# Optimization experiments

Measured on AMD Instinct MI355X. Metric: run time of the kernel, lower is better.

Reference implementation:

```python
import jax, jax.numpy as jnp
import numpy as np

D_MODEL = 1024
NUM_HEADS = 16
D_LATENT = 256
HEAD_DIM = D_MODEL // NUM_HEADS
B, S = 4, 2048


def setup_inputs() -> dict:
    key = jax.random.key(0)
    ks = jax.random.split(key, 11)
    sc_m = 1.0 / np.sqrt(D_MODEL)
    sc_l = 1.0 / np.sqrt(D_LATENT)
    return {
        "x": jax.random.normal(ks[0], (B, S, D_MODEL), dtype=jnp.float32),
        # weights stored as (in, out); equivalent to torch Linear with W^T
        "Wc": jax.random.normal(ks[1], (D_MODEL, D_LATENT), dtype=jnp.float32) * sc_m,
        "bc": jax.random.normal(ks[2], (D_LATENT,), dtype=jnp.float32) * sc_m,
        "Wk": jax.random.normal(ks[3], (D_LATENT, D_MODEL), dtype=jnp.float32) * sc_l,
        "bk": jax.random.normal(ks[4], (D_MODEL,), dtype=jnp.float32) * sc_l,
        "Wv": jax.random.normal(ks[5], (D_LATENT, D_MODEL), dtype=jnp.float32) * sc_l,
        "bv": jax.random.normal(ks[6], (D_MODEL,), dtype=jnp.float32) * sc_l,
        "Wq": jax.random.normal(ks[7], (D_MODEL, D_MODEL), dtype=jnp.float32) * sc_m,
        "bq": jax.random.normal(ks[8], (D_MODEL,), dtype=jnp.float32) * sc_m,
        "Wo": jax.random.normal(ks[9], (D_MODEL, D_MODEL), dtype=jnp.float32) * sc_m,
        "bo": jax.random.normal(ks[10], (D_MODEL,), dtype=jnp.float32) * sc_m,
    }


def reference(x, Wc, bc, Wk, bk, Wv, bv, Wq, bq, Wo, bo):
    b, s, _ = x.shape
    Q = x @ Wq + bq                       # [b,s,d_model]
    kv_latent = x @ Wc + bc               # [b,s,d_latent]
    K = kv_latent @ Wk + bk               # [b,s,d_model]
    V = kv_latent @ Wv + bv               # [b,s,d_model]
    # split heads -> [b,h,s,hd]
    Q = Q.reshape(b, s, NUM_HEADS, HEAD_DIM).transpose(0, 2, 1, 3)
    K = K.reshape(b, s, NUM_HEADS, HEAD_DIM).transpose(0, 2, 1, 3)
    V = V.reshape(b, s, NUM_HEADS, HEAD_DIM).transpose(0, 2, 1, 3)
    scores = jnp.einsum("bhqd,bhkd->bhqk", Q, K) / np.sqrt(HEAD_DIM)
    attn = jax.nn.softmax(scores, axis=-1)  # dropout p=0.0 (eval) -> identity
    out = jnp.einsum("bhqk,bhkd->bhqd", attn, V)
    out = out.transpose(0, 2, 1, 3).reshape(b, s, D_MODEL)
    return out @ Wo + bo
```

## Files before the change

kernel.cpp:

```cpp
#include <hip/hip_runtime.h>

typedef __bf16 bf16;
typedef __bf16 bf16x4 __attribute__((ext_vector_type(4)));
typedef __bf16 bf16x8 __attribute__((ext_vector_type(8)));
typedef float f32x4 __attribute__((ext_vector_type(4)));

#define NHEADS 16
#define HDIM 64
#define SEQ 2048
#define BATCH 4
#define DMODEL 1024
#define NTOK (BATCH * SEQ)
#define KVBLK 64
#define QSCALE 0.18033688f
#define C0EXP  -28.853901f

typedef void gvoid __attribute__((address_space(1)));
typedef void lvoid __attribute__((address_space(3)));

__device__ __forceinline__ f32x4 mfma16(bf16x8 a, bf16x8 b, f32x4 c) {
  return __builtin_amdgcn_mfma_f32_16x16x32_bf16(a, b, c, 0, 0, 0);
}

__device__ __forceinline__ void gload16(const bf16* g, bf16* l) {
  __builtin_amdgcn_global_load_lds((gvoid*)g, (lvoid*)l, 16, 0, 0);
}

__global__ __launch_bounds__(256) void cvt_f32_bf16(
    const float* __restrict__ in, bf16* __restrict__ out, long n) {
  const long i = ((long)blockIdx.x * 256 + threadIdx.x) * 8;
  if (i >= n) return;
  const float4 a = *(const float4*)(in + i);
  const float4 b = *(const float4*)(in + i + 4);
  bf16x8 o;
  o[0] = (bf16)a.x; o[1] = (bf16)a.y; o[2] = (bf16)a.z; o[3] = (bf16)a.w;
  o[4] = (bf16)b.x; o[5] = (bf16)b.y; o[6] = (bf16)b.z; o[7] = (bf16)b.w;
  *(bf16x8*)(out + i) = o;
}

__global__ __launch_bounds__(256) void transpose_cvt(
    const float* __restrict__ in, bf16* __restrict__ out, int K, int N) {
  __shared__ float t[32][33];
  const int n0 = blockIdx.x * 32, k0 = blockIdx.y * 32;
  for (int i = threadIdx.y; i < 32; i += 8)
    t[i][threadIdx.x] = in[(long)(k0 + i) * N + n0 + threadIdx.x];
  __syncthreads();
  for (int i = threadIdx.y; i < 32; i += 8)
    out[(long)(n0 + i) * K + k0 + threadIdx.x] = (bf16)t[threadIdx.x][i];
}

template <int MODE, typename OutT>
__global__ __launch_bounds__(256) void gemm_bt(
    const bf16* __restrict__ A, const bf16* __restrict__ Bt,
    const float* __restrict__ bias, const float* __restrict__ bias2,
    OutT* __restrict__ D, bf16* __restrict__ D2, int N, int K) {
  __shared__ bf16 As[3][128 * 32];
  __shared__ bf16 Bs[3][128 * 32];
  const int tid = threadIdx.x;
  const int lane = tid & 63;
  const int wave = tid >> 6;
  const int wr = (wave >> 1) * 64;
  const int wc = (wave & 1) * 64;
  const int r16 = lane & 15;
  const int kg = lane >> 4;
  const long rowBase = (long)blockIdx.x * 128;
  const long colBase = (long)blockIdx.y * 128;

  const int o0 = tid * 16;
  const int o1 = o0 + 4096;
  const int ra0 = o0 >> 6, ra1 = o1 >> 6;
  const int ca0 = ((o0 & 63) ^ (((ra0 >> 1) & 3) << 4)) >> 1;
  const int ca1 = ((o1 & 63) ^ (((ra1 >> 1) & 3) << 4)) >> 1;
  const bf16* pA0 = A + (rowBase + ra0) * K + ca0;
  const bf16* pA1 = A + (rowBase + ra1) * K + ca1;
  const bf16* pB0 = Bt + (colBase + ra0) * K + ca0;
  const bf16* pB1 = Bt + (colBase + ra1) * K + ca1;
  const int e0 = o0 >> 1, e1 = o1 >> 1;

  auto gaddr = [](const bf16* base, int row, int bytecol) -> const bf16* {
    return base + row * 32 + ((bytecol ^ (((row >> 1) & 3) << 4)) >> 1);
  };

  f32x4 acc[4][4] = {};
  const int nk = K >> 5;

#define GSTAGE(kt_)                                        \
  {                                                        \
    const int b_ = (kt_) % 3;                              \
    const int o_ = (kt_) * 32;                             \
    gload16(pA0 + o_, &As[b_][e0]);                        \
    gload16(pA1 + o_, &As[b_][e1]);                        \
    gload16(pB0 + o_, &Bs[b_][e0]);                        \
    gload16(pB1 + o_, &Bs[b_][e1]);                        \
  }

  GSTAGE(0);
  GSTAGE(1);
  asm volatile("s_waitcnt vmcnt(4)" ::: "memory");
  asm volatile("s_barrier" ::: "memory");

  for (int kt = 0; kt < nk; ++kt) {
    if (kt + 2 < nk) {
      GSTAGE(kt + 2);
      asm volatile("s_waitcnt vmcnt(4)" ::: "memory");
    } else {
      asm volatile("s_waitcnt vmcnt(0)" ::: "memory");
    }
    const bf16* as = As[kt % 3];
    const bf16* bs = Bs[kt % 3];
    bf16x8 af[4], bfr[4];
#pragma unroll
    for (int m = 0; m < 4; ++m)
      af[m] = *(const bf16x8*)gaddr(as, wr + m * 16 + r16, kg * 16);
#pragma unroll
    for (int n = 0; n < 4; ++n)
      bfr[n] = *(const bf16x8*)gaddr(bs, wc + n * 16 + r16, kg * 16);
    __builtin_amdgcn_s_setprio(1);
#pragma unroll
    for (int m = 0; m < 4; ++m)
#pragma unroll
      for (int n = 0; n < 4; ++n)
        acc[m][n] = mfma16(af[m], bfr[n], acc[m][n]);
    __builtin_amdgcn_s_setprio(0);
    asm volatile("s_barrier" ::: "memory");
  }
#undef GSTAGE

#pragma unroll
  for (int n = 0; n < 4; ++n) {
    const long col = colBase + wc + n * 16 + r16;
    const bool primary = (MODE == 0) || (col < 1024);
    const float bvv = primary ? bias[col] : bias2[col - 1024];
#pragma unroll
    for (int m = 0; m < 4; ++m) {
      const long row0 = rowBase + wr + m * 16 + kg * 4;
#pragma unroll
      for (int r = 0; r < 4; ++r) {
        const long row = row0 + r;
        float v = acc[m][n][r] + bvv;
        if (MODE == 0) {
          D[row * N + col] = (OutT)v;
        } else {
          const long b = row >> 11, s = row & (SEQ - 1);
          if (MODE == 3) {
            if (primary) {
              const long h = col >> 6, d = col & 63;
              D[((b * NHEADS + h) * SEQ + s) * HDIM + d] = (OutT)(v * QSCALE);
            } else {
              D2[row * 256 + (col - 1024)] = (bf16)v;
            }
          } else {
            if (primary) {
              const long h = col >> 6, d = col & 63;
              D[((b * NHEADS + h) * SEQ + s) * HDIM + d] = (OutT)v;
            } else {
              const long c2 = col - 1024;
              const long h = c2 >> 6, d = c2 & 63;
              D2[((b * NHEADS + h) * HDIM + d) * SEQ + s] = (bf16)v;
            }
          }
        }
      }
    }
  }
}

__global__ __launch_bounds__(512, 4) void mla_attn(
    const bf16* __restrict__ Q, const bf16* __restrict__ Kg,
    const bf16* __restrict__ Vt, bf16* __restrict__ Out) {
  __shared__ bf16 Kl[3][KVBLK * HDIM];
  __shared__ bf16 Vl[3][HDIM * KVBLK];
  __shared__ bf16 Pl[8][32][64];
  const int tid = threadIdx.x;
  const int lane = tid & 63;
  const int w = tid >> 6;
  const int r16 = lane & 15;
  const int kg = lane >> 4;
  const int bid = (int)blockIdx.x;
  const int lb = (bid & 7) * 64 + (bid >> 3);
  const int qb = lb & 7;
  const int bh = lb >> 3;
  const bf16* Qp = Q + (long)bh * SEQ * HDIM;
  const bf16* Kp = Kg + (long)bh * SEQ * HDIM;
  const bf16* Vp = Vt + (long)bh * HDIM * SEQ;
  const int q0 = qb * 256 + w * 32;

  const int so = tid * 16;
  const int srow = so >> 7;
  const int scol = ((so & 127) ^ ((srow & 7) << 4)) >> 1;
  const bf16* KgS = Kp + (long)srow * HDIM + scol;
  const bf16* VgS = Vp + (long)srow * SEQ + scol;
  const int se = so >> 1;

  bf16x8 aq[2][2];
#pragma unroll
  for (int qm = 0; qm < 2; ++qm) {
    const bf16* qp = Qp + (long)(q0 + qm * 16 + r16) * HDIM + kg * 8;
    aq[qm][0] = *(const bf16x8*)qp;
    aq[qm][1] = *(const bf16x8*)(qp + 32);
  }

  bf16x8 kones;
#pragma unroll
  for (int j = 0; j < 8; ++j) kones[j] = (bf16)1.0f;

  f32x4 accO[2][4];
  f32x4 lsumv[2] = {{0.f, 0.f, 0.f, 0.f}, {0.f, 0.f, 0.f, 0.f}};
#pragma unroll
  for (int qm = 0; qm < 2; ++qm)
#pragma unroll
    for (int dt = 0; dt < 4; ++dt) accO[qm][dt] = (f32x4){0.f, 0.f, 0.f, 0.f};
  const f32x4 c0v = {C0EXP, C0EXP, C0EXP, C0EXP};

  auto kaddr = [](const bf16* base, int row, int bytecol) -> const bf16* {
    return base + row * 64 + ((bytecol ^ ((row & 7) << 4)) >> 1);
  };

#define ASTAGE(t_)                                                   \
  {                                                                  \
    const int b_ = (t_) % 3;                                         \
    const long off_ = (long)(t_) * KVBLK;                            \
    gload16(KgS + off_ * HDIM, (bf16*)Kl[b_] + se);                  \
    gload16(VgS + off_, (bf16*)Vl[b_] + se);                         \
  }

  ASTAGE(0);
  ASTAGE(1);
  asm volatile("s_waitcnt vmcnt(2)" ::: "memory");
  asm volatile("s_barrier" ::: "memory");

  const int NT = SEQ / KVBLK;
  for (int t = 0; t < NT; ++t) {
    if (t + 2 < NT) {
      ASTAGE(t + 2);
      asm volatile("s_waitcnt vmcnt(2)" ::: "memory");
    } else {
      asm volatile("s_waitcnt vmcnt(0)" ::: "memory");
    }
    const bf16* kl = Kl[t % 3];
    const bf16* vl = Vl[t % 3];
    f32x4 sc[2][4];
    __builtin_amdgcn_s_setprio(1);
#pragma unroll
    for (int kt = 0; kt < 4; ++kt) {
      const int row = kt * 16 + r16;
      const bf16x8 kf0 = *(const bf16x8*)kaddr(kl, row, kg * 16);
      const bf16x8 kf1 = *(const bf16x8*)kaddr(kl, row, 64 + kg * 16);
#pragma unroll
      for (int qm = 0; qm < 2; ++qm) {
        f32x4 tv = mfma16(kf0, aq[qm][0], c0v);
        tv = mfma16(kf1, aq[qm][1], tv);
        sc[qm][kt] = tv;
      }
    }
    __builtin_amdgcn_s_setprio(0);
#pragma unroll
    for (int qm = 0; qm < 2; ++qm) {
      bf16* prow = &Pl[w][qm * 16 + r16][0];
      const int sw = (r16 & 7) << 4;
#pragma unroll
      for (int kt = 0; kt < 4; ++kt) {
        bf16x4 pk;
#pragma unroll
        for (int r = 0; r < 4; ++r)
          pk[r] = (bf16)__builtin_amdgcn_exp2f(sc[qm][kt][r]);
        *(bf16x4*)((char*)prow + ((kt * 32 + kg * 8) ^ sw)) = pk;
      }
    }
    __builtin_amdgcn_s_setprio(1);
#pragma unroll
    for (int kc = 0; kc < 2; ++kc) {
      bf16x8 ap[2];
#pragma unroll
      for (int qm = 0; qm < 2; ++qm) {
        const bf16* prow = &Pl[w][qm * 16 + r16][0];
        const int sw = (r16 & 7) << 4;
        ap[qm] = *(const bf16x8*)((const char*)prow + ((kc * 64 + kg * 16) ^ sw));
      }
      lsumv[0] = mfma16(ap[0], kones, lsumv[0]);
      lsumv[1] = mfma16(ap[1], kones, lsumv[1]);
#pragma unroll
      for (int dt = 0; dt < 4; ++dt) {
        const int vrow = dt * 16 + r16;
        const bf16x8 vf = *(const bf16x8*)kaddr(vl, vrow, kc * 64 + kg * 16);
        accO[0][dt] = mfma16(ap[0], vf, accO[0][dt]);
        accO[1][dt] = mfma16(ap[1], vf, accO[1][dt]);
      }
    }
    __builtin_amdgcn_s_setprio(0);
    asm volatile("s_barrier" ::: "memory");
  }
#undef ASTAGE

  const int b = bh >> 4, h = bh & 15;
#pragma unroll
  for (int qm = 0; qm < 2; ++qm)
#pragma unroll
    for (int r = 0; r < 4; ++r) {
      const float inv = 1.f / lsumv[qm][r];
      const long qrow = q0 + qm * 16 + kg * 4 + r;
      bf16* op = Out + ((long)b * SEQ + qrow) * DMODEL + h * HDIM;
#pragma unroll
      for (int dt = 0; dt < 4; ++dt)
        op[dt * 16 + r16] = (bf16)(accO[qm][dt][r] * inv);
    }
}

extern "C" void kernel_launch(void* const* d_in, const int* in_sizes, int n_in,
                              void* d_out, int out_size, void* d_ws, size_t ws_size,
                              hipStream_t stream) {
  const float* x  = (const float*)d_in[0];
  const float* Wc = (const float*)d_in[1];
  const float* bc = (const float*)d_in[2];
  const float* Wk = (const float*)d_in[3];
  const float* bk = (const float*)d_in[4];
  const float* Wv = (const float*)d_in[5];
  const float* bv = (const float*)d_in[6];
  const float* Wq = (const float*)d_in[7];
  const float* bq = (const float*)d_in[8];
  const float* Wo = (const float*)d_in[9];
  const float* bo = (const float*)d_in[10];
  float* out = (float*)d_out;

  bf16* p = (bf16*)d_ws;
  bf16* xb   = p; p += (long)NTOK * 1024;
  bf16* WqcT = p; p += 1280 * 1024;
  bf16* WkvT = p; p += 2048 * 256;
  bf16* WoT  = p; p += 1024 * 1024;
  bf16* Qb   = p; p += (long)NTOK * 1024;
  bf16* Kb   = p; p += (long)NTOK * 1024;
  bf16* Vtb  = p; p += (long)NTOK * 1024;
  bf16* Cb   = p; p += (long)NTOK * 256;
  bf16* AO   = xb;

  cvt_f32_bf16<<<(long)NTOK * 1024 / (256 * 8), 256, 0, stream>>>(x, xb, (long)NTOK * 1024);

  dim3 tt(32, 8);
  transpose_cvt<<<dim3(32, 32), tt, 0, stream>>>(Wq, WqcT, 1024, 1024);
  transpose_cvt<<<dim3(8, 32),  tt, 0, stream>>>(Wc, WqcT + 1024 * 1024, 1024, 256);
  transpose_cvt<<<dim3(32, 8),  tt, 0, stream>>>(Wk, WkvT, 256, 1024);
  transpose_cvt<<<dim3(32, 8),  tt, 0, stream>>>(Wv, WkvT + 1024 * 256, 256, 1024);
  transpose_cvt<<<dim3(32, 32), tt, 0, stream>>>(Wo, WoT, 1024, 1024);

  gemm_bt<3, bf16><<<dim3(64, 10), 256, 0, stream>>>(xb, WqcT, bq, bc, Qb, Cb, 1280, 1024);
  gemm_bt<4, bf16><<<dim3(64, 16), 256, 0, stream>>>(Cb, WkvT, bk, bv, Kb, Vtb, 2048, 256);

  mla_attn<<<(SEQ / 256) * BATCH * NHEADS, 512, 0, stream>>>(Qb, Kb, Vtb, AO);

  gemm_bt<0, float><<<dim3(64, 8), 256, 0, stream>>>(AO, WoT, bo, bo, out, (bf16*)nullptr, 1024, 1024);
}
```

Before: 186.2 us.

## Stage GEMM epilogue through LDS for coalesced stores; sum softmax in registers

The GEMM epilogue for the head-split modes now writes the bias-added tile into shared memory (transposed for the V-transpose output) and then issues coalesced 16-byte row stores, replacing scattered 2-byte global writes. The attention kernel drops the MFMA-with-ones row-sum and instead accumulates fp32 exp values per lane, reducing across lanes with shuffles at the end. This cuts uncoalesced write traffic and MFMA work, at the cost of an extra barrier and LDS pass in the epilogue. The row sum now uses unrounded fp32 values rather than bf16-rounded ones, so the normalization differs slightly.

```diff
diff --git a/kernel.cpp b/kernel.cpp
--- a/kernel.cpp
+++ b/kernel.cpp
@@ -54,8 +54,9 @@
     const bf16* __restrict__ A, const bf16* __restrict__ Bt,
     const float* __restrict__ bias, const float* __restrict__ bias2,
     OutT* __restrict__ D, bf16* __restrict__ D2, int N, int K) {
-  __shared__ bf16 As[3][128 * 32];
-  __shared__ bf16 Bs[3][128 * 32];
+  __shared__ bf16 smem[3 * 4096 * 2];
+  bf16* const AsB = smem;
+  bf16* const BsB = smem + 3 * 4096;
   const int tid = threadIdx.x;
   const int lane = tid & 63;
   const int wave = tid >> 6;
@@ -88,10 +89,10 @@
   {                                                        \
     const int b_ = (kt_) % 3;                              \
     const int o_ = (kt_) * 32;                             \
-    gload16(pA0 + o_, &As[b_][e0]);                        \
-    gload16(pA1 + o_, &As[b_][e1]);                        \
-    gload16(pB0 + o_, &Bs[b_][e0]);                        \
-    gload16(pB1 + o_, &Bs[b_][e1]);                        \
+    gload16(pA0 + o_, AsB + b_ * 4096 + e0);               \
+    gload16(pA1 + o_, AsB + b_ * 4096 + e1);               \
+    gload16(pB0 + o_, BsB + b_ * 4096 + e0);               \
+    gload16(pB1 + o_, BsB + b_ * 4096 + e1);               \
   }
 
   GSTAGE(0);
@@ -106,8 +107,8 @@
     } else {
       asm volatile("s_waitcnt vmcnt(0)" ::: "memory");
     }
-    const bf16* as = As[kt % 3];
-    const bf16* bs = Bs[kt % 3];
+    const bf16* as = AsB + (kt % 3) * 4096;
+    const bf16* bs = BsB + (kt % 3) * 4096;
     bf16x8 af[4], bfr[4];
 #pragma unroll
     for (int m = 0; m < 4; ++m)
@@ -126,42 +127,64 @@
   }
 #undef GSTAGE
 
-#pragma unroll
-  for (int n = 0; n < 4; ++n) {
-    const long col = colBase + wc + n * 16 + r16;
-    const bool primary = (MODE == 0) || (col < 1024);
-    const float bvv = primary ? bias[col] : bias2[col - 1024];
-#pragma unroll
-    for (int m = 0; m < 4; ++m) {
-      const long row0 = rowBase + wr + m * 16 + kg * 4;
-#pragma unroll
-      for (int r = 0; r < 4; ++r) {
-        const long row = row0 + r;
-        float v = acc[m][n][r] + bvv;
-        if (MODE == 0) {
-          D[row * N + col] = (OutT)v;
-        } else {
-          const long b = row >> 11, s = row & (SEQ - 1);
-          if (MODE == 3) {
-            if (primary) {
-              const long h = col >> 6, d = col & 63;
-              D[((b * NHEADS + h) * SEQ + s) * HDIM + d] = (OutT)(v * QSCALE);
-            } else {
-              D2[row * 256 + (col - 1024)] = (bf16)v;
-            }
-          } else {
-            if (primary) {
-              const long h = col >> 6, d = col & 63;
-              D[((b * NHEADS + h) * SEQ + s) * HDIM + d] = (OutT)v;
-            } else {
-              const long c2 = col - 1024;
-              const long h = c2 >> 6, d = c2 & 63;
-              D2[((b * NHEADS + h) * HDIM + d) * SEQ + s] = (bf16)v;
-            }
-          }
+  if (MODE == 0) {
+#pragma unroll
+    for (int n = 0; n < 4; ++n) {
+      const long col = colBase + wc + n * 16 + r16;
+      const float bvv = bias[col];
+#pragma unroll
+      for (int m = 0; m < 4; ++m) {
+        const long row0 = rowBase + wr + m * 16 + kg * 4;
+#pragma unroll
+        for (int r = 0; r < 4; ++r)
+          D[(row0 + r) * N + col] = (OutT)(acc[m][n][r] + bvv);
+      }
+    }
+  } else {
+    const bool tr = (MODE == 4) && (colBase >= 1024);
+    bf16* E = smem;
+#pragma unroll
+    for (int n = 0; n < 4; ++n) {
+      const int cl = wc + n * 16 + r16;
+      const long col = colBase + cl;
+      const bool primary = col < 1024;
+      const float bvv = primary ? bias[col] : bias2[col - 1024];
+#pragma unroll
+      for (int m = 0; m < 4; ++m) {
+#pragma unroll
+        for (int r = 0; r < 4; ++r) {
+          const int rl = wr + m * 16 + kg * 4 + r;
+          float v = acc[m][n][r] + bvv;
+          if (MODE == 3 && primary) v *= QSCALE;
+          if (tr) E[cl * 136 + rl] = (bf16)v;
+          else    E[rl * 136 + cl] = (bf16)v;
         }
       }
     }
+    __syncthreads();
+    const int er = tid >> 1;
+    const int c0 = (tid & 1) * 64;
+    const long brow = rowBase >> 11;
+    const int srow = (int)(rowBase & 2047);
+    bf16* dp;
+    if (!tr) {
+      if (colBase < 1024) {
+        const long col = colBase + c0;
+        dp = D2, dp = nullptr;
+        dp = (bf16*)(void*)D +
+             (((brow * NHEADS + (col >> 6)) * SEQ) + srow + er) * HDIM;
+      } else {
+        dp = D2 + (long)(rowBase + er) * 256 + (colBase - 1024) + c0;
+      }
+    } else {
+      const long c2 = colBase - 1024 + er;
+      dp = D2 + ((brow * NHEADS + (c2 >> 6)) * HDIM + (c2 & 63)) * SEQ +
+           srow + c0;
+    }
+    const bf16* Er = E + er * 136 + c0;
+#pragma unroll
+    for (int j = 0; j < 8; ++j)
+      *(bf16x8*)(dp + j * 8) = *(const bf16x8*)(Er + j * 8);
   }
 }
 
@@ -200,12 +223,8 @@
     aq[qm][1] = *(const bf16x8*)(qp + 32);
   }
 
-  bf16x8 kones;
-#pragma unroll
-  for (int j = 0; j < 8; ++j) kones[j] = (bf16)1.0f;
-
   f32x4 accO[2][4];
-  f32x4 lsumv[2] = {{0.f, 0.f, 0.f, 0.f}, {0.f, 0.f, 0.f, 0.f}};
+  float psum[2] = {0.f, 0.f};
 #pragma unroll
   for (int qm = 0; qm < 2; ++qm)
 #pragma unroll
@@ -262,8 +281,11 @@
       for (int kt = 0; kt < 4; ++kt) {
         bf16x4 pk;
 #pragma unroll
-        for (int r = 0; r < 4; ++r)
-          pk[r] = (bf16)__builtin_amdgcn_exp2f(sc[qm][kt][r]);
+        for (int r = 0; r < 4; ++r) {
+          const float pv = __builtin_amdgcn_exp2f(sc[qm][kt][r]);
+          pk[r] = (bf16)pv;
+          psum[qm] += pv;
+        }
         *(bf16x4*)((char*)prow + ((kt * 32 + kg * 8) ^ sw)) = pk;
       }
     }
@@ -277,8 +299,6 @@
         const int sw = (r16 & 7) << 4;
         ap[qm] = *(const bf16x8*)((const char*)prow + ((kc * 64 + kg * 16) ^ sw));
       }
-      lsumv[0] = mfma16(ap[0], kones, lsumv[0]);
-      lsumv[1] = mfma16(ap[1], kones, lsumv[1]);
 #pragma unroll
       for (int dt = 0; dt < 4; ++dt) {
         const int vrow = dt * 16 + r16;
@@ -292,12 +312,17 @@
   }
 #undef ASTAGE
 
+#pragma unroll
+  for (int qm = 0; qm < 2; ++qm) {
+    psum[qm] += __shfl_xor(psum[qm], 16);
+    psum[qm] += __shfl_xor(psum[qm], 32);
+  }
   const int b = bh >> 4, h = bh & 15;
 #pragma unroll
   for (int qm = 0; qm < 2; ++qm)
 #pragma unroll
     for (int r = 0; r < 4; ++r) {
-      const float inv = 1.f / lsumv[qm][r];
+      const float inv = 1.f / __shfl(psum[qm], kg * 4 + r);
       const long qrow = q0 + qm * 16 + kg * 4 + r;
       bf16* op = Out + ((long)b * SEQ + qrow) * DMODEL + h * HDIM;
 #pragma unroll
```

After: 185.9 us. About the same (-0.2%).
